# Performance work log

Measured on AMD Instinct MI355X. Metric: run time of the kernel, lower is better.

The kernel has to match this reference:

```python
import jax, jax.numpy as jnp
import numpy as np

N_NODES = 50000
N_EDGES = 800000
C = 64          # node channels (in_dim == out_dim)
CE = 32         # edge channels
NEG_SLOPE = 0.2


def setup_inputs() -> dict:
    key = jax.random.key(0)
    k1, k2, k3, k4, k5 = jax.random.split(key, 5)
    x = jax.random.normal(k1, (N_NODES, C), dtype=jnp.float32)
    edge_index = jax.random.randint(k2, (2, N_EDGES), 0, N_NODES, dtype=jnp.int64)
    edge_attr = jax.random.normal(k3, (N_EDGES, CE), dtype=jnp.float32)
    # parameters (kaiming-uniform-ish scale)
    wn_bound = float(np.sqrt(6.0 / C))
    weight_node = jax.random.uniform(k4, (C, C), minval=-wn_bound, maxval=wn_bound, dtype=jnp.float32)
    wa_bound = float(np.sqrt(6.0 / (2 * C + CE)))
    weight_triplet_att = jax.random.uniform(k5, (1, 2 * C + CE), minval=-wa_bound, maxval=wa_bound, dtype=jnp.float32)
    bias = jnp.zeros((C,), dtype=jnp.float32)
    return {"x": x, "edge_index": edge_index, "edge_attr": edge_attr,
            "weight_node": weight_node, "weight_triplet_att": weight_triplet_att, "bias": bias}


def reference(x, edge_index, edge_attr, weight_node, weight_triplet_att, bias):
    # x: [N, C], edge_index: [2, E] (row 0 = source j, row 1 = target i), edge_attr: [E, Ce]
    n_nodes = x.shape[0]
    xw = x @ weight_node                      # [N, C]
    src, dst = edge_index[0], edge_index[1]
    x_j = xw[src]                             # [E, C] messages from source
    x_i = xw[dst]                             # [E, C] target features
    triplet = jnp.concatenate([x_i, edge_attr, x_j], axis=-1)   # [E, 2C+Ce]
    alpha = (triplet * weight_triplet_att).sum(axis=-1)          # [E]
    alpha = jax.nn.leaky_relu(alpha, NEG_SLOPE)
    # segment softmax over edges grouped by destination node (PyG softmax)
    seg_max = jax.ops.segment_max(alpha, dst, num_segments=n_nodes)  # [N]
    alpha = jnp.exp(alpha - seg_max[dst])
    seg_sum = jax.ops.segment_sum(alpha, dst, num_segments=n_nodes)  # [N]
    alpha = alpha / (seg_sum[dst] + 1e-16)
    msg = alpha[:, None] * x_j                                      # [E, C]
    out = jax.ops.segment_sum(msg, dst, num_segments=n_nodes)       # [N, C]
    return out + bias
```

## Files before the change

kernel.cpp:

```cpp
#include <hip/hip_runtime.h>
#include <math.h>

#define N_NODES 50000
#define N_EDGES 800000
#define C 64
#define CE 32
#define NEG_SLOPE 0.2f

#define SCAN_BLOCK 256
#define SCAN_ELEMS 4
#define SCAN_TILE (SCAN_BLOCK * SCAN_ELEMS)
#define SCAN_SHIFT 10
#define SCAN_NBLOCKS ((N_NODES + SCAN_TILE - 1) / SCAN_TILE)

__device__ __forceinline__ unsigned bf16_rne(float f) {
    unsigned u = __float_as_uint(f);
    return (u + 0x7FFFu + ((u >> 16) & 1u)) >> 16;
}

__global__ __launch_bounds__(256) void k1_xw(
    const float* __restrict__ x, const float* __restrict__ W,
    const float* __restrict__ watt,
    unsigned short* __restrict__ xwb, float* __restrict__ a_i, float* __restrict__ a_j)
{
    __shared__ float Wl[64 * 64];
    __shared__ float xs[4][64];
    int tid = threadIdx.x;
    for (int i = tid; i < 64 * 64 / 4; i += 256)
        ((float4*)Wl)[i] = ((const float4*)W)[i];
    int warp = tid >> 6, lane = tid & 63;
    int row = blockIdx.x * 4 + warp;
    if (row < N_NODES) xs[warp][lane] = x[(size_t)row * C + lane];
    __syncthreads();
    if (row >= N_NODES) return;
    float acc = 0.f;
#pragma unroll
    for (int k = 0; k < 64; k++) acc += xs[warp][k] * Wl[k * 64 + lane];
    xwb[(size_t)row * C + lane] = (unsigned short)bf16_rne(acc);
    float vi = acc * watt[lane];
    float vj = acc * watt[96 + lane];
#pragma unroll
    for (int off = 32; off; off >>= 1) {
        vi += __shfl_down(vi, off, 64);
        vj += __shfl_down(vj, off, 64);
    }
    if (lane == 0) { a_i[row] = vi; a_j[row] = vj; }
}

__global__ __launch_bounds__(256) void k2_edge(
    const int* __restrict__ eidx, const float* __restrict__ edge_attr,
    const float* __restrict__ watt,
    const float* __restrict__ a_i, const float* __restrict__ a_j,
    unsigned* __restrict__ packA, unsigned* __restrict__ packB,
    unsigned* __restrict__ count)
{
    int tid = threadIdx.x;
    int lane = tid & 63;
    int sub = tid & 7;
    int e = (blockIdx.x * 256 + tid) >> 3;
    if (e >= N_EDGES) return;
    float4 v = ((const float4*)edge_attr)[(size_t)e * (CE / 4) + sub];
    float4 wv = ((const float4*)(watt + 64))[sub];
    float p = v.x * wv.x + v.y * wv.y + v.z * wv.z + v.w * wv.w;
    p += __shfl_xor(p, 1, 64);
    p += __shfl_xor(p, 2, 64);
    p += __shfl_xor(p, 4, 64);
    float myec = __shfl(p, (lane & 7) * 8, 64);
    if (lane < 8) {
        int eg = ((blockIdx.x * 256 + (tid & ~63)) >> 3) + lane;
        if (eg < N_EDGES) {
            int src = eidx[eg];
            int dst = eidx[N_EDGES + eg];
            float al = a_i[dst] + myec + a_j[src];
            al = al > 0.f ? al : NEG_SLOPE * al;
            packA[eg] = ((unsigned)src << 16) | bf16_rne(__expf(al));
            unsigned r = atomicAdd(&count[dst], 1u);
            packB[eg] = ((unsigned)dst << 16) | r;
        }
    }
}

__global__ __launch_bounds__(SCAN_BLOCK) void k3a_blockscan(
    const unsigned* __restrict__ count, unsigned* __restrict__ base,
    unsigned* __restrict__ blocksum)
{
    __shared__ unsigned wsum[4];
    int tid = threadIdx.x, lane = tid & 63, warp = tid >> 6;
    int gbase = blockIdx.x * SCAN_TILE + tid * SCAN_ELEMS;
    unsigned v[SCAN_ELEMS];
    unsigned s = 0;
#pragma unroll
    for (int k = 0; k < SCAN_ELEMS; k++) {
        int i = gbase + k;
        v[k] = (i < N_NODES) ? count[i] : 0u;
        s += v[k];
    }
    unsigned inc = s;
#pragma unroll
    for (int off = 1; off < 64; off <<= 1) {
        unsigned t = __shfl_up(inc, off, 64);
        if (lane >= off) inc += t;
    }
    if (lane == 63) wsum[warp] = inc;
    __syncthreads();
    unsigned wpre = 0;
#pragma unroll
    for (int w = 0; w < 4; w++) if (w < warp) wpre += wsum[w];
    unsigned run = wpre + inc - s;
#pragma unroll
    for (int k = 0; k < SCAN_ELEMS; k++) {
        int i = gbase + k;
        if (i < N_NODES) base[i] = run;
        run += v[k];
    }
    if (tid == 255) blocksum[blockIdx.x] = wpre + inc;
}

__global__ __launch_bounds__(64) void k3b_scansums(unsigned* __restrict__ blocksum)
{
    int lane = threadIdx.x;
    unsigned v = (lane < SCAN_NBLOCKS) ? blocksum[lane] : 0u;
    unsigned inc = v;
#pragma unroll
    for (int off = 1; off < 64; off <<= 1) {
        unsigned t = __shfl_up(inc, off, 64);
        if (lane >= off) inc += t;
    }
    if (lane < SCAN_NBLOCKS) blocksum[lane] = inc - v;
}

__global__ __launch_bounds__(256) void k4_scatter(
    const unsigned* __restrict__ packA, const unsigned* __restrict__ packB,
    const unsigned* __restrict__ base, const unsigned* __restrict__ blocksum,
    unsigned* __restrict__ sorted)
{
    int e = blockIdx.x * 256 + threadIdx.x;
    if (e >= N_EDGES) return;
    unsigned pa = packA[e];
    unsigned pb = packB[e];
    unsigned d = pb >> 16;
    sorted[base[d] + blocksum[d >> SCAN_SHIFT] + (pb & 0xFFFFu)] = pa;
}

__global__ __launch_bounds__(256) void k5_gather(
    const unsigned* __restrict__ base, const unsigned* __restrict__ blocksum,
    const unsigned* __restrict__ count, const unsigned* __restrict__ sorted,
    const unsigned short* __restrict__ xwb, const float* __restrict__ bias,
    float* __restrict__ out)
{
    int warp = threadIdx.x >> 6, lane = threadIdx.x & 63;
    int node = blockIdx.x * 4 + warp;
    if (node >= N_NODES) return;
    int group = lane >> 3, sub = lane & 7;
    unsigned b = base[node] + blocksum[(unsigned)node >> SCAN_SHIFT];
    unsigned c = count[node];
    float acc[8];
#pragma unroll
    for (int i = 0; i < 8; i++) acc[i] = 0.f;
    float wpart = 0.f;
    for (unsigned chunk = 0; chunk < c; chunk += 64) {
        unsigned m = min(64u, c - chunk);
        unsigned pk = 0u;
        if (lane < m) pk = sorted[b + chunk + lane];
        wpart += __uint_as_float(pk << 16);
        unsigned iters = (m + 7) >> 3;
        for (unsigned it = 0; it < iters; it++) {
            int t = (int)(it * 8) + group;
            unsigned p = (unsigned)__shfl((int)pk, t, 64);
            float w = __uint_as_float(p << 16);
            unsigned s = p >> 16;
            uint4 v = ((const uint4*)(xwb + (size_t)s * C))[sub];
            acc[0] += w * __uint_as_float(v.x << 16);
            acc[1] += w * __uint_as_float(v.x & 0xFFFF0000u);
            acc[2] += w * __uint_as_float(v.y << 16);
            acc[3] += w * __uint_as_float(v.y & 0xFFFF0000u);
            acc[4] += w * __uint_as_float(v.z << 16);
            acc[5] += w * __uint_as_float(v.z & 0xFFFF0000u);
            acc[6] += w * __uint_as_float(v.w << 16);
            acc[7] += w * __uint_as_float(v.w & 0xFFFF0000u);
        }
    }
#pragma unroll
    for (int off = 8; off < 64; off <<= 1) {
#pragma unroll
        for (int i = 0; i < 8; i++) acc[i] += __shfl_xor(acc[i], off, 64);
    }
#pragma unroll
    for (int off = 1; off < 64; off <<= 1)
        wpart += __shfl_xor(wpart, off, 64);
    float rden = 1.0f / (wpart + 1e-16f);
    if (group == 0) {
        float4 b4a = ((const float4*)bias)[sub * 2];
        float4 b4b = ((const float4*)bias)[sub * 2 + 1];
        float4 o1, o2;
        o1.x = acc[0] * rden + b4a.x; o1.y = acc[1] * rden + b4a.y;
        o1.z = acc[2] * rden + b4a.z; o1.w = acc[3] * rden + b4a.w;
        o2.x = acc[4] * rden + b4b.x; o2.y = acc[5] * rden + b4b.y;
        o2.z = acc[6] * rden + b4b.z; o2.w = acc[7] * rden + b4b.w;
        ((float4*)(out + (size_t)node * C))[sub * 2] = o1;
        ((float4*)(out + (size_t)node * C))[sub * 2 + 1] = o2;
    }
}

extern "C" void kernel_launch(void* const* d_in, const int* in_sizes, int n_in,
                              void* d_out, int out_size, void* d_ws, size_t ws_size,
                              hipStream_t stream) {
    const float* x         = (const float*)d_in[0];
    const int*   eidx      = (const int*)d_in[1];
    const float* edge_attr = (const float*)d_in[2];
    const float* W         = (const float*)d_in[3];
    const float* watt      = (const float*)d_in[4];
    const float* bias      = (const float*)d_in[5];
    float* out = (float*)d_out;

    char* ws = (char*)d_ws;
    size_t off = 0;
    auto alloc = [&](size_t bytes) -> void* {
        void* p = ws + off;
        off += (bytes + 255) & ~(size_t)255;
        return p;
    };
    unsigned short* xwb = (unsigned short*)alloc((size_t)N_NODES * C * 2);
    float*    a_i      = (float*)alloc(N_NODES * 4);
    float*    a_j      = (float*)alloc(N_NODES * 4);
    unsigned* packA    = (unsigned*)alloc(N_EDGES * 4);
    unsigned* packB    = (unsigned*)alloc(N_EDGES * 4);
    unsigned* sorted   = (unsigned*)alloc((size_t)N_EDGES * 4);
    unsigned* basep    = (unsigned*)alloc(N_NODES * 4);
    unsigned* blocksum = (unsigned*)alloc(SCAN_NBLOCKS * 4);
    unsigned* count    = (unsigned*)alloc(N_NODES * 4);

    hipMemsetAsync(count, 0, (size_t)N_NODES * 4, stream);

    k1_xw<<<(N_NODES + 3) / 4, 256, 0, stream>>>(x, W, watt, xwb, a_i, a_j);
    k2_edge<<<(N_EDGES * 8) / 256, 256, 0, stream>>>(eidx, edge_attr, watt, a_i, a_j,
                                                     packA, packB, count);
    k3a_blockscan<<<SCAN_NBLOCKS, SCAN_BLOCK, 0, stream>>>(count, basep, blocksum);
    k3b_scansums<<<1, 64, 0, stream>>>(blocksum);
    k4_scatter<<<(N_EDGES + 255) / 256, 256, 0, stream>>>(packA, packB, basep,
                                                          blocksum, sorted);
    k5_gather<<<(N_NODES + 3) / 4, 256, 0, stream>>>(basep, blocksum, count, sorted,
                                                     xwb, bias, out);
}
```

Measured before the change: 260.3 us.

## Remap edge and gather kernels to use all lanes, fuse count reset into xw

The edge kernel now has each block handle 256 edges. Edge-attribute dot products are staged in shared memory so all 256 threads do the index, exp and atomic work, instead of only 8 lanes per wave. The gather kernel assigns 8 lanes per node, eight nodes per wave, which removes the wave-wide cross-group reductions and the mostly idle lanes. The count memset is folded into the xw kernel, saving one launch. The risk is lower per-node parallelism for high-degree nodes and more divergence from uneven degrees inside a wave.

```diff
diff --git a/kernel.cpp b/kernel.cpp
--- a/kernel.cpp
+++ b/kernel.cpp
@@ -21,11 +21,16 @@
 __global__ __launch_bounds__(256) void k1_xw(
     const float* __restrict__ x, const float* __restrict__ W,
     const float* __restrict__ watt,
-    unsigned short* __restrict__ xwb, float* __restrict__ a_i, float* __restrict__ a_j)
+    unsigned short* __restrict__ xwb, float* __restrict__ a_i, float* __restrict__ a_j,
+    unsigned* __restrict__ count)
 {
     __shared__ float Wl[64 * 64];
     __shared__ float xs[4][64];
     int tid = threadIdx.x;
+    if (tid < 4) {
+        int n = blockIdx.x * 4 + tid;
+        if (n < N_NODES) count[n] = 0u;
+    }
     for (int i = tid; i < 64 * 64 / 4; i += 256)
         ((float4*)Wl)[i] = ((const float4*)W)[i];
     int warp = tid >> 6, lane = tid & 63;
@@ -54,30 +59,30 @@
     unsigned* __restrict__ packA, unsigned* __restrict__ packB,
     unsigned* __restrict__ count)
 {
+    __shared__ float ecs[256];
     int tid = threadIdx.x;
-    int lane = tid & 63;
     int sub = tid & 7;
-    int e = (blockIdx.x * 256 + tid) >> 3;
-    if (e >= N_EDGES) return;
-    float4 v = ((const float4*)edge_attr)[(size_t)e * (CE / 4) + sub];
+    int e0 = blockIdx.x * 256;
     float4 wv = ((const float4*)(watt + 64))[sub];
-    float p = v.x * wv.x + v.y * wv.y + v.z * wv.z + v.w * wv.w;
-    p += __shfl_xor(p, 1, 64);
-    p += __shfl_xor(p, 2, 64);
-    p += __shfl_xor(p, 4, 64);
-    float myec = __shfl(p, (lane & 7) * 8, 64);
-    if (lane < 8) {
-        int eg = ((blockIdx.x * 256 + (tid & ~63)) >> 3) + lane;
-        if (eg < N_EDGES) {
-            int src = eidx[eg];
-            int dst = eidx[N_EDGES + eg];
-            float al = a_i[dst] + myec + a_j[src];
-            al = al > 0.f ? al : NEG_SLOPE * al;
-            packA[eg] = ((unsigned)src << 16) | bf16_rne(__expf(al));
-            unsigned r = atomicAdd(&count[dst], 1u);
-            packB[eg] = ((unsigned)dst << 16) | r;
-        }
-    }
+#pragma unroll
+    for (int pass = 0; pass < 8; pass++) {
+        int le = pass * 32 + (tid >> 3);
+        float4 v = ((const float4*)edge_attr)[(size_t)(e0 + le) * (CE / 4) + sub];
+        float p = v.x * wv.x + v.y * wv.y + v.z * wv.z + v.w * wv.w;
+        p += __shfl_xor(p, 1, 64);
+        p += __shfl_xor(p, 2, 64);
+        p += __shfl_xor(p, 4, 64);
+        if (sub == 0) ecs[le] = p;
+    }
+    __syncthreads();
+    int e = e0 + tid;
+    int src = eidx[e];
+    int dst = eidx[N_EDGES + e];
+    float al = a_i[dst] + ecs[tid] + a_j[src];
+    al = al > 0.f ? al : NEG_SLOPE * al;
+    packA[e] = ((unsigned)src << 16) | bf16_rne(__expf(al));
+    unsigned r = atomicAdd(&count[dst], 1u);
+    packB[e] = ((unsigned)dst << 16) | r;
 }
 
 __global__ __launch_bounds__(SCAN_BLOCK) void k3a_blockscan(
@@ -148,25 +153,24 @@
     const unsigned short* __restrict__ xwb, const float* __restrict__ bias,
     float* __restrict__ out)
 {
-    int warp = threadIdx.x >> 6, lane = threadIdx.x & 63;
-    int node = blockIdx.x * 4 + warp;
+    int tid = threadIdx.x;
+    int wave = tid >> 6, lane = tid & 63;
+    int g = lane >> 3, sub = lane & 7;
+    int node = (blockIdx.x * 4 + wave) * 8 + g;
     if (node >= N_NODES) return;
-    int group = lane >> 3, sub = lane & 7;
     unsigned b = base[node] + blocksum[(unsigned)node >> SCAN_SHIFT];
     unsigned c = count[node];
     float acc[8];
 #pragma unroll
     for (int i = 0; i < 8; i++) acc[i] = 0.f;
     float wpart = 0.f;
-    for (unsigned chunk = 0; chunk < c; chunk += 64) {
-        unsigned m = min(64u, c - chunk);
+    for (unsigned i0 = 0; i0 < c; i0 += 8) {
+        unsigned m = min(8u, c - i0);
         unsigned pk = 0u;
-        if (lane < m) pk = sorted[b + chunk + lane];
+        if (sub < m) pk = sorted[b + i0 + sub];
         wpart += __uint_as_float(pk << 16);
-        unsigned iters = (m + 7) >> 3;
-        for (unsigned it = 0; it < iters; it++) {
-            int t = (int)(it * 8) + group;
-            unsigned p = (unsigned)__shfl((int)pk, t, 64);
+        for (unsigned it = 0; it < m; it++) {
+            unsigned p = (unsigned)__shfl((int)pk, g * 8 + (int)it, 64);
             float w = __uint_as_float(p << 16);
             unsigned s = p >> 16;
             uint4 v = ((const uint4*)(xwb + (size_t)s * C))[sub];
@@ -180,26 +184,19 @@
             acc[7] += w * __uint_as_float(v.w & 0xFFFF0000u);
         }
     }
-#pragma unroll
-    for (int off = 8; off < 64; off <<= 1) {
-#pragma unroll
-        for (int i = 0; i < 8; i++) acc[i] += __shfl_xor(acc[i], off, 64);
-    }
-#pragma unroll
-    for (int off = 1; off < 64; off <<= 1)
-        wpart += __shfl_xor(wpart, off, 64);
+    wpart += __shfl_xor(wpart, 1, 64);
+    wpart += __shfl_xor(wpart, 2, 64);
+    wpart += __shfl_xor(wpart, 4, 64);
     float rden = 1.0f / (wpart + 1e-16f);
-    if (group == 0) {
-        float4 b4a = ((const float4*)bias)[sub * 2];
-        float4 b4b = ((const float4*)bias)[sub * 2 + 1];
-        float4 o1, o2;
-        o1.x = acc[0] * rden + b4a.x; o1.y = acc[1] * rden + b4a.y;
-        o1.z = acc[2] * rden + b4a.z; o1.w = acc[3] * rden + b4a.w;
-        o2.x = acc[4] * rden + b4b.x; o2.y = acc[5] * rden + b4b.y;
-        o2.z = acc[6] * rden + b4b.z; o2.w = acc[7] * rden + b4b.w;
-        ((float4*)(out + (size_t)node * C))[sub * 2] = o1;
-        ((float4*)(out + (size_t)node * C))[sub * 2 + 1] = o2;
-    }
+    float4 b4a = ((const float4*)bias)[sub * 2];
+    float4 b4b = ((const float4*)bias)[sub * 2 + 1];
+    float4 o1, o2;
+    o1.x = acc[0] * rden + b4a.x; o1.y = acc[1] * rden + b4a.y;
+    o1.z = acc[2] * rden + b4a.z; o1.w = acc[3] * rden + b4a.w;
+    o2.x = acc[4] * rden + b4b.x; o2.y = acc[5] * rden + b4b.y;
+    o2.z = acc[6] * rden + b4b.z; o2.w = acc[7] * rden + b4b.w;
+    ((float4*)(out + (size_t)node * C))[sub * 2] = o1;
+    ((float4*)(out + (size_t)node * C))[sub * 2 + 1] = o2;
 }
 
 extern "C" void kernel_launch(void* const* d_in, const int* in_sizes, int n_in,
@@ -230,15 +227,13 @@
     unsigned* blocksum = (unsigned*)alloc(SCAN_NBLOCKS * 4);
     unsigned* count    = (unsigned*)alloc(N_NODES * 4);
 
-    hipMemsetAsync(count, 0, (size_t)N_NODES * 4, stream);
-
-    k1_xw<<<(N_NODES + 3) / 4, 256, 0, stream>>>(x, W, watt, xwb, a_i, a_j);
-    k2_edge<<<(N_EDGES * 8) / 256, 256, 0, stream>>>(eidx, edge_attr, watt, a_i, a_j,
-                                                     packA, packB, count);
+    k1_xw<<<(N_NODES + 3) / 4, 256, 0, stream>>>(x, W, watt, xwb, a_i, a_j, count);
+    k2_edge<<<N_EDGES / 256, 256, 0, stream>>>(eidx, edge_attr, watt, a_i, a_j,
+                                               packA, packB, count);
     k3a_blockscan<<<SCAN_NBLOCKS, SCAN_BLOCK, 0, stream>>>(count, basep, blocksum);
     k3b_scansums<<<1, 64, 0, stream>>>(blocksum);
     k4_scatter<<<(N_EDGES + 255) / 256, 256, 0, stream>>>(packA, packB, basep,
                                                           blocksum, sorted);
-    k5_gather<<<(N_NODES + 3) / 4, 256, 0, stream>>>(basep, blocksum, count, sorted,
-                                                     xwb, bias, out);
-}
+    k5_gather<<<(N_NODES / 32) + 1, 256, 0, stream>>>(basep, blocksum, count, sorted,
+                                                      xwb, bias, out);
+}
```

Result: no change. 265.3 us (+1.9%).
